# Performance work log

Measured on AMD Instinct MI355X. Metric: run time of the kernel, lower is better.

The kernel has to match this reference:

```python
import jax, jax.numpy as jnp
import numpy as np

NUM_HEADS = 12
SEQ_H = 32
SEQ_W = 32
D_HALF = 32
ROPE_BASE = 10000.0
LN_EPS = 1e-5


def build_rope_cache(seq_len, head_dim, base=ROPE_BASE):
    inv_freq = 1.0 / base ** (jnp.arange(0, head_dim, 2, dtype=jnp.float32) / head_dim)
    t = jnp.arange(seq_len, dtype=jnp.float32)
    freqs = jnp.outer(t, inv_freq)  # [seq_len, head_dim//2]
    cos = jnp.repeat(jnp.cos(freqs), 2, axis=-1)  # [seq_len, head_dim]
    sin = jnp.repeat(jnp.sin(freqs), 2, axis=-1)
    return cos, sin


def apply_rope(x, cos, sin):
    # x: [B,H,N,d_sub], cos/sin: [N,d_sub]
    x_even, x_odd = x[..., ::2], x[..., 1::2]
    x_rot = jnp.stack([-x_odd, x_even], axis=-1).reshape(x.shape)
    return x * cos[None, None] + x_rot * sin[None, None]


def setup_inputs() -> dict:
    key = jax.random.key(0)
    ks = jax.random.split(key, 3)
    B, N, D = 8, 1025, 768
    return {
        "x": jax.random.normal(ks[0], (B, N, D), dtype=jnp.float32),
        "ln_g": jnp.ones((D,), dtype=jnp.float32),
        "ln_b": jnp.zeros((D,), dtype=jnp.float32),
        "w_qkv": jax.random.normal(ks[1], (3 * D, D), dtype=jnp.float32) * 0.02,
        "w_proj": jax.random.normal(ks[2], (D, D), dtype=jnp.float32) * 0.02,
        "b_proj": jnp.zeros((D,), dtype=jnp.float32),
    }


def reference(x, ln_g, ln_b, w_qkv, w_proj, b_proj):
    B, N, D = x.shape
    H = NUM_HEADS
    hd = D // H
    d2 = D_HALF
    scale = hd ** -0.5

    # LayerNorm
    mu = jnp.mean(x, axis=-1, keepdims=True)
    var = jnp.mean(jnp.square(x - mu), axis=-1, keepdims=True)
    xn = (x - mu) * jax.lax.rsqrt(var + LN_EPS) * ln_g + ln_b

    # QKV projection (no bias)
    qkv = jnp.einsum("bnd,ed->bne", xn, w_qkv).reshape(B, N, 3, H, hd)
    qkv = jnp.transpose(qkv, (2, 0, 3, 1, 4))  # [3,B,H,N,hd]
    q, k, v = qkv[0], qkv[1], qkv[2]

    # 2D position ids (CLS token -> row 0, col 0)
    patch_lin = jnp.arange(N - 1)
    rows = patch_lin // SEQ_W
    cols = patch_lin % SEQ_W
    zero = jnp.zeros((1,), dtype=patch_lin.dtype)
    row_ids = jnp.concatenate([zero, rows])
    col_ids = jnp.concatenate([zero, cols])

    cos_row, sin_row = build_rope_cache(SEQ_H, d2)
    cos_col, sin_col = build_rope_cache(SEQ_W, d2)
    cos_r, sin_r = cos_row[row_ids], sin_row[row_ids]  # [N,d2]
    cos_c, sin_c = cos_col[col_ids], sin_col[col_ids]

    q = jnp.concatenate(
        [apply_rope(q[..., :d2], cos_r, sin_r), apply_rope(q[..., d2:], cos_c, sin_c)], axis=-1)
    k = jnp.concatenate(
        [apply_rope(k[..., :d2], cos_r, sin_r), apply_rope(k[..., d2:], cos_c, sin_c)], axis=-1)

    attn = jnp.einsum("bhqd,bhkd->bhqk", q, k) * scale
    attn = jax.nn.softmax(attn, axis=-1)
    out = jnp.einsum("bhqk,bhkd->bhqd", attn, v)  # [B,H,N,hd]
    out = jnp.transpose(out, (0, 2, 1, 3)).reshape(B, N, D)
    return jnp.einsum("bnd,ed->bne", out, w_proj) + b_proj
```

## Files before the change

### kernel.cpp

```cpp
#include <hip/hip_runtime.h>
#include <hip/hip_bf16.h>

typedef unsigned short u16;

#define B_      8
#define N_      1025
#define D_      768
#define H_      12
#define HD_     64
#define M_REAL  (B_ * N_)
#define M_PAD   8320
#define QKVC    (3 * D_)

typedef __attribute__((ext_vector_type(8))) short bf16x8;
typedef __attribute__((ext_vector_type(4))) float f32x4;

static __device__ __forceinline__ float bf2f(u16 u) {
    union { unsigned int i; float f; } v; v.i = ((unsigned int)u) << 16; return v.f;
}
static __device__ __forceinline__ u16 f2bf(float f) {
    union { float f; unsigned int i; } v; v.f = f;
    unsigned int x = v.i;
    return (u16)((x + 0x7fffu + ((x >> 16) & 1u)) >> 16);
}
static __device__ __forceinline__ unsigned int cvtpk(float a, float b) {
    unsigned int r;
    asm volatile("v_cvt_pk_bf16_f32 %0, %1, %2" : "=v"(r) : "v"(a), "v"(b));
    return r;
}

static __device__ __forceinline__ void g2l16(const u16* g, u16* l) {
    __builtin_amdgcn_global_load_lds(
        (const __attribute__((address_space(1))) unsigned int*)g,
        (__attribute__((address_space(3))) unsigned int*)l, 16, 0, 0);
}

__global__ __launch_bounds__(256)
void ln_f2b_kernel(const float* __restrict__ x, const float* __restrict__ g,
                   const float* __restrict__ bvec, u16* __restrict__ xn,
                   const float* __restrict__ wq, u16* __restrict__ wqb,
                   const float* __restrict__ wp, u16* __restrict__ wpb)
{
    const int tid = threadIdx.x;
    if (blockIdx.x >= M_REAL) {
        int i = (blockIdx.x - M_REAL) * 1024 + tid * 4;
        const float* src; u16* dst;
        if (i < QKVC * D_) { src = wq + i; dst = wqb + i; }
        else { src = wp + (i - QKVC * D_); dst = wpb + (i - QKVC * D_); }
        float4 v = *(const float4*)src;
        dst[0] = f2bf(v.x); dst[1] = f2bf(v.y);
        dst[2] = f2bf(v.z); dst[3] = f2bf(v.w);
        return;
    }
    const int row = blockIdx.x;
    const float* xr = x + (size_t)row * D_;
    float v[3];
    float s = 0.f, ss = 0.f;
#pragma unroll
    for (int j = 0; j < 3; j++) {
        float val = xr[tid + j * 256];
        v[j] = val; s += val; ss += val * val;
    }
    __shared__ float r1[256], r2[256];
    r1[tid] = s; r2[tid] = ss; __syncthreads();
    for (int off = 128; off > 0; off >>= 1) {
        if (tid < off) { r1[tid] += r1[tid + off]; r2[tid] += r2[tid + off]; }
        __syncthreads();
    }
    const float mean = r1[0] * (1.0f / D_);
    const float var  = r2[0] * (1.0f / D_) - mean * mean;
    const float rs   = rsqrtf(var + 1e-5f);
    u16* outr = xn + (size_t)row * D_;
#pragma unroll
    for (int j = 0; j < 3; j++) {
        int c = tid + j * 256;
        outr[c] = f2bf((v[j] - mean) * rs * g[c] + bvec[c]);
    }
}

template <typename OutT, bool ROPE>
__global__ __launch_bounds__(256)
void gemm_bt(const u16* __restrict__ A, const u16* __restrict__ B,
             OutT* __restrict__ C, const float* __restrict__ bias,
             int M_real, int Ncols, int K,
             int BM, int BN, int gh, int gw, int PC)
{
    const int l   = blockIdx.x;
    const int xcd = l & 7;
    const int i0  = l >> 3;
    const int pr  = xcd / PC, pc = xcd % PC;
    const int bm  = pr * gh + (i0 % gh);
    const int bn  = pc * gw + (i0 / gh);
    if (bm >= BM || bn >= BN) return;

    __shared__ __align__(16) unsigned char smem[34816];
    u16* As0 = (u16*)smem;
    u16* Bs0 = (u16*)(smem + 8192);
    u16*   ep16 = (u16*)smem;
    float* ep32 = (float*)smem;

    const int tid  = threadIdx.x;
    const int wave = tid >> 6, lane = tid & 63;
    const int wm   = (wave >> 1) * 64, wn = (wave & 1) * 64;
    const int lrow = lane & 15, lq = lane >> 4;
    const int lrow4 = lane >> 2, lchunk = lane & 3;

    int ar0 = bm * 128 + wave * 16 + lrow4;       if (ar0 >= M_real) ar0 = M_real - 1;
    int ar1 = bm * 128 + (wave + 4) * 16 + lrow4; if (ar1 >= M_real) ar1 = M_real - 1;
    const u16* apg0 = A + (size_t)ar0 * K + lchunk * 8;
    const u16* apg1 = A + (size_t)ar1 * K + lchunk * 8;
    const u16* bpg0 = B + (size_t)(bn * 128 + wave * 16 + lrow4) * K + lchunk * 8;
    const u16* bpg1 = B + (size_t)(bn * 128 + (wave + 4) * 16 + lrow4) * K + lchunk * 8;
    u16* asl0 = As0 + wave * 512;       u16* asl1 = As0 + (wave + 4) * 512;
    u16* bsl0 = Bs0 + wave * 512;       u16* bsl1 = Bs0 + (wave + 4) * 512;
    const int bufoff = 8192;

    f32x4 acc[4][4];
#pragma unroll
    for (int i = 0; i < 4; i++)
#pragma unroll
        for (int j = 0; j < 4; j++)
            acc[i][j] = (f32x4){0.f, 0.f, 0.f, 0.f};

    g2l16(apg0, asl0); g2l16(apg1, asl1);
    g2l16(bpg0, bsl0); g2l16(bpg1, bsl1);

    const int kTiles = K / 32;
    for (int kt = 0; kt < kTiles; kt++) {
        const int cur = kt & 1;
        __syncthreads();
        if (kt + 1 < kTiles) {
            const int k1 = (kt + 1) * 32;
            const int no = (cur ^ 1) * bufoff;
            g2l16(apg0 + k1, asl0 + no); g2l16(apg1 + k1, asl1 + no);
            g2l16(bpg0 + k1, bsl0 + no); g2l16(bpg1 + k1, bsl1 + no);
        }
        const u16* Asr = As0 + cur * bufoff;
        const u16* Bsr = Bs0 + cur * bufoff;
        bf16x8 af[4], bfr[4];
#pragma unroll
        for (int i = 0; i < 4; i++) {
            af[i]  = *(const bf16x8*)&Asr[(wm + i * 16 + lrow) * 32 + lq * 8];
            bfr[i] = *(const bf16x8*)&Bsr[(wn + i * 16 + lrow) * 32 + lq * 8];
        }
#pragma unroll
        for (int i = 0; i < 4; i++)
#pragma unroll
            for (int j = 0; j < 4; j++)
                acc[i][j] = __builtin_amdgcn_mfma_f32_16x16x32_bf16(af[i], bfr[j], acc[i][j], 0, 0, 0);
    }
    __syncthreads();

    if constexpr (sizeof(OutT) == 2) {
#pragma unroll
        for (int j = 0; j < 4; j++) {
            int gcol = bn * 128 + wn + j * 16 + lrow;
            float bv = bias ? bias[gcol] : 0.f;
            int qk = gcol / D_;
            int dh = gcol & 63;
            int half = dh >> 5, ii = (dh & 31) >> 1;
            float sgn = (dh & 1) ? 1.f : -1.f;
            float invf = exp2f(-(float)ii * 0.8304820237218406f);
#pragma unroll
            for (int i = 0; i < 4; i++)
#pragma unroll
                for (int r = 0; r < 4; r++) {
                    int grow = bm * 128 + wm + i * 16 + lq * 4 + r;
                    float val = acc[i][j][r] + bv;
                    if constexpr (ROPE) {
                        if (qk < 2) {
                            float partner = __shfl_xor(val, 1);
                            int n = grow % N_;
                            int pl = n - 1;
                            int pos = (n == 0) ? 0 : (half ? (pl & 31) : (pl >> 5));
                            float ang = (float)pos * invf;
                            val = val * __cosf(ang) + sgn * partner * __sinf(ang);
                            if (qk == 0) val *= 0.125f;
                        }
                    }
                    ep16[(wm + i * 16 + lq * 4 + r) * 136 + wn + j * 16 + lrow] = f2bf(val);
                }
        }
        __syncthreads();
#pragma unroll
        for (int c = 0; c < 8; c++) {
            int idx = tid + c * 256;
            int row = idx >> 4, l16 = idx & 15;
            int grow = bm * 128 + row;
            if (grow < M_real)
                *(uint4*)((u16*)C + (size_t)grow * Ncols + bn * 128 + l16 * 8) =
                    *(const uint4*)&ep16[row * 136 + l16 * 8];
        }
    } else {
#pragma unroll
        for (int s = 0; s < 2; s++) {
            if (s) __syncthreads();
            if (wm == s * 64) {
#pragma unroll
                for (int j = 0; j < 4; j++) {
                    int gcol = bn * 128 + wn + j * 16 + lrow;
                    float bv = bias ? bias[gcol] : 0.f;
#pragma unroll
                    for (int i = 0; i < 4; i++)
#pragma unroll
                        for (int r = 0; r < 4; r++)
                            ep32[(i * 16 + lq * 4 + r) * 132 + wn + j * 16 + lrow] =
                                acc[i][j][r] + bv;
                }
            }
            __syncthreads();
#pragma unroll
            for (int c = 0; c < 8; c++) {
                int idx = tid + c * 256;
                int row = idx >> 5, l32 = idx & 31;
                int grow = bm * 128 + s * 64 + row;
                if (grow < M_real)
                    *(uint4*)((float*)C + (size_t)grow * Ncols + bn * 128 + l32 * 4) =
                        *(const uint4*)&ep32[row * 132 + l32 * 4];
            }
        }
    }
}

__global__ __launch_bounds__(256)
void attn_mfma(const u16* __restrict__ qkv, u16* __restrict__ out)
{
    __shared__ __align__(16) u16 Vt[2][64][72];
    __shared__ float Lw[4][32];

    const int l   = blockIdx.x;
    const int xcd = l & 7;
    const int j0  = l >> 3;
    const int bh  = xcd * 12 + j0 / 9;
    const int b  = bh / H_, h = bh % H_;
    const int q0 = (j0 % 9) * 128;
    const int tid  = threadIdx.x;
    const int wave = tid >> 6, lane = tid & 63;
    const int lm = lane & 15, lq = lane >> 4;
    const int qw = q0 + wave * 32;

    const int vcol = (lane & 35) | ((lane & 12) << 1) | ((lane & 16) >> 2);

    bf16x8 qf[2][2];
#pragma unroll
    for (int sq = 0; sq < 2; sq++) {
        int qrow = qw + sq * 16 + lm; if (qrow > N_ - 1) qrow = N_ - 1;
        const u16* qptr = qkv + (size_t)(b * N_ + qrow) * QKVC + h * HD_;
        qf[sq][0] = *(const bf16x8*)(qptr + lq * 8);
        qf[sq][1] = *(const bf16x8*)(qptr + 32 + lq * 8);
    }

    const u16* kb_ptr = qkv + (size_t)b * N_ * QKVC + D_ + h * HD_ + lq * 8;
    const u16* vb_ptr = qkv + (size_t)b * N_ * QKVC + 2 * D_ + h * HD_ + wave * 8;

    float l_r[2] = {0.f, 0.f};
    f32x4 o_acc[2][4];
#pragma unroll
    for (int sq = 0; sq < 2; sq++)
#pragma unroll
        for (int t = 0; t < 4; t++)
            o_acc[sq][t] = (f32x4){0.f, 0.f, 0.f, 0.f};

    bf16x8 kf[4][2], vreg[2];
#pragma unroll
    for (int st = 0; st < 4; st++) {
        const u16* p = kb_ptr + (size_t)(st * 16 + lm) * QKVC;
        kf[st][0] = *(const bf16x8*)p;
        kf[st][1] = *(const bf16x8*)(p + 32);
    }
    {
        const u16* p = vb_ptr + (size_t)lane * QKVC;
        vreg[0] = *(const bf16x8*)p;
        vreg[1] = *(const bf16x8*)(p + 32);
    }

    const int kTiles = (N_ + 63) / 64;
    for (int kt = 0; kt < kTiles; kt++) {
        const int kbase = kt * 64;
        const int buf = kt & 1;

#pragma unroll
        for (int pp = 0; pp < 2; pp++) {
            int dg = wave + pp * 4;
#pragma unroll
            for (int j = 0; j < 8; j++)
                Vt[buf][dg * 8 + j][vcol] = (u16)vreg[pp][j];
        }

        f32x4 sc[2][4];
        __builtin_amdgcn_s_setprio(1);
#pragma unroll
        for (int st = 0; st < 4; st++)
#pragma unroll
            for (int sq = 0; sq < 2; sq++) {
                f32x4 s4 = (f32x4){0.f, 0.f, 0.f, 0.f};
                s4 = __builtin_amdgcn_mfma_f32_16x16x32_bf16(kf[st][0], qf[sq][0], s4, 0, 0, 0);
                s4 = __builtin_amdgcn_mfma_f32_16x16x32_bf16(kf[st][1], qf[sq][1], s4, 0, 0, 0);
                sc[sq][st] = s4;
            }
        __builtin_amdgcn_s_setprio(0);

        if (kt + 1 < kTiles) {
            const int kb = kbase + 64;
#pragma unroll
            for (int st = 0; st < 4; st++) {
                int kr = kb + st * 16 + lm; if (kr > N_ - 1) kr = N_ - 1;
                const u16* p = kb_ptr + (size_t)kr * QKVC;
                kf[st][0] = *(const bf16x8*)p;
                kf[st][1] = *(const bf16x8*)(p + 32);
            }
            int kr = kb + lane; if (kr > N_ - 1) kr = N_ - 1;
            const u16* p = vb_ptr + (size_t)kr * QKVC;
            vreg[0] = *(const bf16x8*)p;
            vreg[1] = *(const bf16x8*)(p + 32);
        }

        asm volatile("s_waitcnt lgkmcnt(0)" ::: "memory");
        __builtin_amdgcn_s_barrier();

        const bool lastT = (kt == kTiles - 1);
        bf16x8 pa[2][2];
#pragma unroll
        for (int sq = 0; sq < 2; sq++) {
            union { bf16x8 v; unsigned int u[4]; } pk0, pk1;
#pragma unroll
            for (int st = 0; st < 4; st++) {
                float p0 = __expf(sc[sq][st][0]);
                float p1 = __expf(sc[sq][st][1]);
                float p2 = __expf(sc[sq][st][2]);
                float p3 = __expf(sc[sq][st][3]);
                if (lastT) {
                    const int keyb = kbase + st * 16 + lq * 4;
                    if (keyb + 0 >= N_) p0 = 0.f;
                    if (keyb + 1 >= N_) p1 = 0.f;
                    if (keyb + 2 >= N_) p2 = 0.f;
                    if (keyb + 3 >= N_) p3 = 0.f;
                }
                l_r[sq] += (p0 + p1) + (p2 + p3);
                unsigned int lo = cvtpk(p0, p1);
                unsigned int hi = cvtpk(p2, p3);
                if      (st == 0) { pk0.u[0] = lo; pk0.u[1] = hi; }
                else if (st == 1) { pk0.u[2] = lo; pk0.u[3] = hi; }
                else if (st == 2) { pk1.u[0] = lo; pk1.u[1] = hi; }
                else              { pk1.u[2] = lo; pk1.u[3] = hi; }
            }
            pa[sq][0] = pk0.v; pa[sq][1] = pk1.v;
        }

        __builtin_amdgcn_s_setprio(1);
#pragma unroll
        for (int nt = 0; nt < 4; nt++) {
            bf16x8 vb0 = *(const bf16x8*)&Vt[buf][nt * 16 + lm][lq * 8];
            bf16x8 vb1 = *(const bf16x8*)&Vt[buf][nt * 16 + lm][32 + lq * 8];
#pragma unroll
            for (int sq = 0; sq < 2; sq++) {
                o_acc[sq][nt] = __builtin_amdgcn_mfma_f32_16x16x32_bf16(pa[sq][0], vb0, o_acc[sq][nt], 0, 0, 0);
                o_acc[sq][nt] = __builtin_amdgcn_mfma_f32_16x16x32_bf16(pa[sq][1], vb1, o_acc[sq][nt], 0, 0, 0);
            }
        }
        __builtin_amdgcn_s_setprio(0);
    }

#pragma unroll
    for (int sq = 0; sq < 2; sq++) {
        float l2 = l_r[sq];
        l2 += __shfl_xor(l2, 16);
        l2 += __shfl_xor(l2, 32);
        if (lq == 0) Lw[wave][sq * 16 + lm] = l2;
    }
    asm volatile("s_waitcnt lgkmcnt(0)" ::: "memory");

#pragma unroll
    for (int sq = 0; sq < 2; sq++)
#pragma unroll
        for (int r = 0; r < 4; r++) {
            int q = qw + sq * 16 + lq * 4 + r;
            if (q < N_) {
                float inv = 1.0f / Lw[wave][sq * 16 + lq * 4 + r];
                u16* orow = out + (size_t)(b * N_ + q) * D_ + h * HD_ + lm;
#pragma unroll
                for (int nt = 0; nt < 4; nt++)
                    orow[nt * 16] = f2bf(o_acc[sq][nt][r] * inv);
            }
        }
}

extern "C" void kernel_launch(void* const* d_in, const int* in_sizes, int n_in,
                              void* d_out, int out_size, void* d_ws, size_t ws_size,
                              hipStream_t stream)
{
    const float* x      = (const float*)d_in[0];
    const float* ln_g   = (const float*)d_in[1];
    const float* ln_b   = (const float*)d_in[2];
    const float* w_qkv  = (const float*)d_in[3];
    const float* w_proj = (const float*)d_in[4];
    const float* b_proj = (const float*)d_in[5];

    u16* wqkv_b  = (u16*)d_ws;
    u16* wproj_b = wqkv_b + (size_t)QKVC * D_;
    u16* xn      = wproj_b + (size_t)D_ * D_;
    u16* qkv     = xn + (size_t)M_PAD * D_;
    u16* attno   = xn;

    ln_f2b_kernel<<<M_REAL + (QKVC * D_ + D_ * D_) / 1024, 256, 0, stream>>>(
        x, ln_g, ln_b, xn, w_qkv, wqkv_b, w_proj, wproj_b);

    gemm_bt<u16, true><<<1224, 256, 0, stream>>>(
        xn, wqkv_b, qkv, nullptr, M_REAL, QKVC, D_,
        65, 18, 17, 9, 2);

    attn_mfma<<<864, 256, 0, stream>>>(qkv, attno);

    gemm_bt<float, false><<<432, 256, 0, stream>>>(
        attno, wproj_b, (float*)d_out, b_proj, M_REAL, D_, D_,
        65, 6, 9, 6, 1);
}
```

Baseline: 247.0 us.

## Stage K tiles through shared memory instead of per-wave global loads

Each wave used to load the full 64-key K tile straight from global memory into registers, so all four waves fetched the same K data. Now every thread loads one slice of K alongside V, writes it into a double-buffered LDS tile, and after a barrier the waves read their MFMA operands from LDS. The goal is to cut redundant global and L2 traffic and register pressure from the K fragments. In exchange it adds LDS writes and reads, and the barrier now sits before the QK MFMAs, which could reduce overlap between compute and loads.

```diff
diff --git a/kernel.cpp b/kernel.cpp
--- a/kernel.cpp
+++ b/kernel.cpp
@@ -225,6 +225,7 @@
 __global__ __launch_bounds__(256)
 void attn_mfma(const u16* __restrict__ qkv, u16* __restrict__ out)
 {
+    __shared__ __align__(16) u16 Kt[2][64][72];
     __shared__ __align__(16) u16 Vt[2][64][72];
     __shared__ float Lw[4][32];
 
@@ -250,9 +251,6 @@
         qf[sq][1] = *(const bf16x8*)(qptr + 32 + lq * 8);
     }
 
-    const u16* kb_ptr = qkv + (size_t)b * N_ * QKVC + D_ + h * HD_ + lq * 8;
-    const u16* vb_ptr = qkv + (size_t)b * N_ * QKVC + 2 * D_ + h * HD_ + wave * 8;
-
     float l_r[2] = {0.f, 0.f};
     f32x4 o_acc[2][4];
 #pragma unroll
@@ -261,17 +259,16 @@
         for (int t = 0; t < 4; t++)
             o_acc[sq][t] = (f32x4){0.f, 0.f, 0.f, 0.f};
 
-    bf16x8 kf[4][2], vreg[2];
-#pragma unroll
-    for (int st = 0; st < 4; st++) {
-        const u16* p = kb_ptr + (size_t)(st * 16 + lm) * QKVC;
-        kf[st][0] = *(const bf16x8*)p;
-        kf[st][1] = *(const bf16x8*)(p + 32);
-    }
+    bf16x8 kreg[2], vreg[2];
     {
-        const u16* p = vb_ptr + (size_t)lane * QKVC;
-        vreg[0] = *(const bf16x8*)p;
-        vreg[1] = *(const bf16x8*)(p + 32);
+        int krow = lane; if (krow > N_ - 1) krow = N_ - 1;
+        const u16* kvp = qkv + (size_t)(b * N_ + krow) * QKVC + h * HD_;
+#pragma unroll
+        for (int p = 0; p < 2; p++) {
+            int dg = wave + p * 4;
+            kreg[p] = *(const bf16x8*)(kvp + D_ + dg * 8);
+            vreg[p] = *(const bf16x8*)(kvp + 2 * D_ + dg * 8);
+        }
     }
 
     const int kTiles = (N_ + 63) / 64;
@@ -282,41 +279,41 @@
 #pragma unroll
         for (int pp = 0; pp < 2; pp++) {
             int dg = wave + pp * 4;
+            *(bf16x8*)&Kt[buf][lane][dg * 8] = kreg[pp];
 #pragma unroll
             for (int j = 0; j < 8; j++)
                 Vt[buf][dg * 8 + j][vcol] = (u16)vreg[pp][j];
         }
 
+        if (kt + 1 < kTiles) {
+            int krow = kbase + 64 + lane; if (krow > N_ - 1) krow = N_ - 1;
+            const u16* kvp = qkv + (size_t)(b * N_ + krow) * QKVC + h * HD_;
+#pragma unroll
+            for (int pp = 0; pp < 2; pp++) {
+                int dg = wave + pp * 4;
+                kreg[pp] = *(const bf16x8*)(kvp + D_ + dg * 8);
+                vreg[pp] = *(const bf16x8*)(kvp + 2 * D_ + dg * 8);
+            }
+        }
+
+        asm volatile("s_waitcnt lgkmcnt(0)" ::: "memory");
+        __builtin_amdgcn_s_barrier();
+
         f32x4 sc[2][4];
         __builtin_amdgcn_s_setprio(1);
 #pragma unroll
-        for (int st = 0; st < 4; st++)
+        for (int st = 0; st < 4; st++) {
+            bf16x8 kf0 = *(const bf16x8*)&Kt[buf][st * 16 + lm][lq * 8];
+            bf16x8 kf1 = *(const bf16x8*)&Kt[buf][st * 16 + lm][32 + lq * 8];
 #pragma unroll
             for (int sq = 0; sq < 2; sq++) {
                 f32x4 s4 = (f32x4){0.f, 0.f, 0.f, 0.f};
-                s4 = __builtin_amdgcn_mfma_f32_16x16x32_bf16(kf[st][0], qf[sq][0], s4, 0, 0, 0);
-                s4 = __builtin_amdgcn_mfma_f32_16x16x32_bf16(kf[st][1], qf[sq][1], s4, 0, 0, 0);
+                s4 = __builtin_amdgcn_mfma_f32_16x16x32_bf16(kf0, qf[sq][0], s4, 0, 0, 0);
+                s4 = __builtin_amdgcn_mfma_f32_16x16x32_bf16(kf1, qf[sq][1], s4, 0, 0, 0);
                 sc[sq][st] = s4;
             }
+        }
         __builtin_amdgcn_s_setprio(0);
-
-        if (kt + 1 < kTiles) {
-            const int kb = kbase + 64;
-#pragma unroll
-            for (int st = 0; st < 4; st++) {
-                int kr = kb + st * 16 + lm; if (kr > N_ - 1) kr = N_ - 1;
-                const u16* p = kb_ptr + (size_t)kr * QKVC;
-                kf[st][0] = *(const bf16x8*)p;
-                kf[st][1] = *(const bf16x8*)(p + 32);
-            }
-            int kr = kb + lane; if (kr > N_ - 1) kr = N_ - 1;
-            const u16* p = vb_ptr + (size_t)kr * QKVC;
-            vreg[0] = *(const bf16x8*)p;
-            vreg[1] = *(const bf16x8*)(p + 32);
-        }
-
-        asm volatile("s_waitcnt lgkmcnt(0)" ::: "memory");
-        __builtin_amdgcn_s_barrier();
 
         const bool lastT = (kt == kTiles - 1);
         bf16x8 pa[2][2];
```

After: 214.7 us. 1.15x faster.
